# Kernel tuning notes

Measured on AMD Instinct MI355X. Metric: run time of the kernel, lower is better.

Reference implementation:

```python
import jax, jax.numpy as jnp
import numpy as np

# Static table layout: first N_NUM columns are numeric ('num:'), last N_CAT are categorical ('cat:').
B = 16384      # rows in the table
N_NUM = 32     # numeric columns
N_CAT = 8      # categorical columns
N_COLS = N_NUM + N_CAT
D = 256        # cell_embedding_dim
C = 16         # num_classes per categorical column = len(values) + 1 = 15 + 1


def setup_inputs() -> dict:
    key = jax.random.key(0)
    ks = jax.random.split(key, 7)
    s = 0.02  # typical init scale for Linear weights
    return {
        "cell_embeddings": jax.random.normal(ks[0], (B * N_COLS, D), dtype=jnp.float32),
        # numeric decoder: Linear(D, 1), stored as [D, 1] (transposed torch weight)
        "w_num": jax.random.normal(ks[1], (D, 1), dtype=jnp.float32) * s,
        "b_num": jnp.zeros((1,), dtype=jnp.float32),
        # categorical decoders: one Linear(D, C) per categorical column, stacked [N_CAT, D, C]
        "W_cat": jax.random.normal(ks[2], (N_CAT, D, C), dtype=jnp.float32) * s,
        "b_cat": jnp.zeros((N_CAT, C), dtype=jnp.float32),
        # missingness decoder: Linear(D, 1)
        "w_miss": jax.random.normal(ks[3], (D, 1), dtype=jnp.float32) * s,
        "b_miss": jnp.zeros((1,), dtype=jnp.float32),
    }


def reference(cell_embeddings, w_num, b_num, W_cat, b_cat, w_miss, b_miss):
    # [B*N_COLS, D] -> [B, N_COLS, D]; column j always routes to the same decoder.
    x = cell_embeddings.reshape(B, N_COLS, D)

    # Numeric cells: shared Linear(D -> 1), batched over all numeric cells.  [B, N_NUM]
    num_preds = (x[:, :N_NUM, :] @ w_num)[..., 0] + b_num[0]

    # Categorical cells: per-column Linear(D -> C), grouped GEMM.  [B, N_CAT, C]
    cat_logits = jnp.einsum('bjd,jdc->bjc', x[:, N_NUM:, :], W_cat) + b_cat

    # Missingness decoder applied to every cell.  [B, N_COLS]
    miss_logits = (x @ w_miss)[..., 0] + b_miss[0]

    return num_preds, cat_logits, miss_logits
```

## Files before the change

### kernel.cpp

```cpp
#include <hip/hip_runtime.h>

constexpr int B_     = 16384;
constexpr int NNUM   = 32;
constexpr int NCAT   = 8;
constexpr int NCOLS  = 40;
constexpr int DD     = 256;
constexpr int CC     = 16;

constexpr int BDIM     = 256;
constexpr int NBLOCKS  = 2048;
constexpr int NWAVES   = NBLOCKS * (BDIM / 64);
constexpr int NW_CAT   = 2048;
constexpr int NW_NUM   = NWAVES - NW_CAT;
constexpr int NUM_CELLS = B_ * NNUM;

constexpr int OUT_NUM_SZ  = B_ * NNUM;
constexpr int OUT_CAT_SZ  = B_ * NCAT * CC;

__global__ __launch_bounds__(BDIM, 4)
void tabdec_kernel(const float* __restrict__ X,
                   const float* __restrict__ w_num,  const float* __restrict__ b_num,
                   const float* __restrict__ W_cat,  const float* __restrict__ b_cat,
                   const float* __restrict__ w_miss, const float* __restrict__ b_miss,
                   float* __restrict__ out_num, float* __restrict__ out_cat,
                   float* __restrict__ out_miss)
{
    const int tid  = blockIdx.x * BDIM + threadIdx.x;
    const int wid  = tid >> 6;
    const int lane = threadIdx.x & 63;
    const float4* __restrict__ Xv = reinterpret_cast<const float4*>(X);

    if (wid < NW_NUM) {
        const float4 wn = reinterpret_cast<const float4*>(w_num)[lane];
        const float4 wm = reinterpret_cast<const float4*>(w_miss)[lane];
        const float bn = b_num[0];
        const float bm = b_miss[0];
        for (int i = 2 * wid; i < NUM_CELLS; i += 2 * NW_NUM) {
            const int b = i >> 5;
            const int j = i & 31;
            const int row0 = b * NCOLS + j;
            const float4 x0 = Xv[row0 * (DD / 4) + lane];
            const float4 x1 = Xv[(row0 + 1) * (DD / 4) + lane];
            float pn0 = x0.x * wn.x + x0.y * wn.y + x0.z * wn.z + x0.w * wn.w;
            float pm0 = x0.x * wm.x + x0.y * wm.y + x0.z * wm.z + x0.w * wm.w;
            float pn1 = x1.x * wn.x + x1.y * wn.y + x1.z * wn.z + x1.w * wn.w;
            float pm1 = x1.x * wm.x + x1.y * wm.y + x1.z * wm.z + x1.w * wm.w;
            #pragma unroll
            for (int m = 1; m < 64; m <<= 1) {
                pn0 += __shfl_xor(pn0, m, 64);
                pn1 += __shfl_xor(pn1, m, 64);
                pm0 += __shfl_xor(pm0, m, 64);
                pm1 += __shfl_xor(pm1, m, 64);
            }
            if (lane == 0) {
                out_num[i]     = pn0 + bn;
                out_num[i + 1] = pn1 + bn;
                out_miss[row0]     = pm0 + bm;
                out_miss[row0 + 1] = pm1 + bm;
            }
        }
    } else {
        const int wc = wid - NW_NUM;
        const int j  = wc >> 8;
        const int b0 = wc & 255;
        const float* Wj = W_cat + j * DD * CC;

        float4 w0[4], w1[4], w2[4], w3[4];
        #pragma unroll
        for (int k = 0; k < 4; ++k) {
            const float4* wr = reinterpret_cast<const float4*>(Wj + (lane * 4 + k) * CC);
            w0[k] = wr[0]; w1[k] = wr[1]; w2[k] = wr[2]; w3[k] = wr[3];
        }
        const float4 wm = reinterpret_cast<const float4*>(w_miss)[lane];
        const float bm = b_miss[0];
        const int cbr = ((lane & 1) << 3) | ((lane & 2) << 1) | ((lane & 4) >> 1) | ((lane & 8) >> 3);
        const float bias = b_cat[j * CC + cbr];
        const bool h1 = lane & 1, h2 = lane & 2, h3 = lane & 4, h4 = lane & 8;

        for (int b = b0; b < B_; b += 256) {
            const int row = b * NCOLS + NNUM + j;
            const float4 x = Xv[row * (DD / 4) + lane];
            const float xe0 = x.x, xe1 = x.y, xe2 = x.z, xe3 = x.w;

            float p[16];
            #pragma unroll
            for (int c = 0; c < 16; ++c) p[c] = 0.0f;
            #define ACC(k, xk) \
                p[0]  += xk * w0[k].x; p[1]  += xk * w0[k].y; p[2]  += xk * w0[k].z; p[3]  += xk * w0[k].w; \
                p[4]  += xk * w1[k].x; p[5]  += xk * w1[k].y; p[6]  += xk * w1[k].z; p[7]  += xk * w1[k].w; \
                p[8]  += xk * w2[k].x; p[9]  += xk * w2[k].y; p[10] += xk * w2[k].z; p[11] += xk * w2[k].w; \
                p[12] += xk * w3[k].x; p[13] += xk * w3[k].y; p[14] += xk * w3[k].z; p[15] += xk * w3[k].w;
            ACC(0, xe0) ACC(1, xe1) ACC(2, xe2) ACC(3, xe3)
            #undef ACC

            float pm = x.x * wm.x + x.y * wm.y + x.z * wm.z + x.w * wm.w;

            float q[8];
            #pragma unroll
            for (int i = 0; i < 8; ++i) {
                const float send = h1 ? p[i] : p[i + 8];
                const float keep = h1 ? p[i + 8] : p[i];
                q[i] = keep + __shfl_xor(send, 1, 64);
            }
            float r[4];
            #pragma unroll
            for (int i = 0; i < 4; ++i) {
                const float send = h2 ? q[i] : q[i + 4];
                const float keep = h2 ? q[i + 4] : q[i];
                r[i] = keep + __shfl_xor(send, 2, 64);
            }
            float s[2];
            #pragma unroll
            for (int i = 0; i < 2; ++i) {
                const float send = h3 ? r[i] : r[i + 2];
                const float keep = h3 ? r[i + 2] : r[i];
                s[i] = keep + __shfl_xor(send, 4, 64);
            }
            {
                const float send = h4 ? s[0] : s[1];
                const float keep = h4 ? s[1] : s[0];
                s[0] = keep + __shfl_xor(send, 8, 64);
            }
            float t = s[0];
            t += __shfl_xor(t, 16, 64);
            t += __shfl_xor(t, 32, 64);

            #pragma unroll
            for (int m = 1; m < 64; m <<= 1) pm += __shfl_xor(pm, m, 64);

            if (lane < 16) out_cat[b * (NCAT * CC) + j * CC + cbr] = t + bias;
            if (lane == 0) out_miss[b * NCOLS + NNUM + j] = pm + bm;
        }
    }
}

extern "C" void kernel_launch(void* const* d_in, const int* in_sizes, int n_in,
                              void* d_out, int out_size, void* d_ws, size_t ws_size,
                              hipStream_t stream) {
    const float* X      = (const float*)d_in[0];
    const float* w_num  = (const float*)d_in[1];
    const float* b_num  = (const float*)d_in[2];
    const float* W_cat  = (const float*)d_in[3];
    const float* b_cat  = (const float*)d_in[4];
    const float* w_miss = (const float*)d_in[5];
    const float* b_miss = (const float*)d_in[6];

    float* out_num  = (float*)d_out;
    float* out_cat  = out_num + OUT_NUM_SZ;
    float* out_miss = out_cat + OUT_CAT_SZ;

    tabdec_kernel<<<NBLOCKS, BDIM, 0, stream>>>(X, w_num, b_num, W_cat, b_cat,
                                                w_miss, b_miss,
                                                out_num, out_cat, out_miss);
}
```

Measured before the change: 891.4 us.

## Split decoder into separate numeric and categorical kernels with packed shuffle reduction

Replaces the single wave-partitioned kernel with two launches: a numeric kernel where each wave handles four cells and packs the num/miss dot products into one shared butterfly shuffle reduction, and a categorical kernel with twice as many waves per column. The aim is to cut shuffle count per cell and remove load imbalance between the two wave groups. In exchange the two phases now run serially on the stream, and the numeric kernel uses higher occupancy bounds.

Measured after the change: 883.0 us. About the same (-0.9%).

```diff
diff --git a/kernel.cpp b/kernel.cpp
--- a/kernel.cpp
+++ b/kernel.cpp
@@ -7,130 +7,153 @@
 constexpr int DD     = 256;
 constexpr int CC     = 16;
 
-constexpr int BDIM     = 256;
-constexpr int NBLOCKS  = 2048;
-constexpr int NWAVES   = NBLOCKS * (BDIM / 64);
-constexpr int NW_CAT   = 2048;
-constexpr int NW_NUM   = NWAVES - NW_CAT;
-constexpr int NUM_CELLS = B_ * NNUM;
-
 constexpr int OUT_NUM_SZ  = B_ * NNUM;
 constexpr int OUT_CAT_SZ  = B_ * NCAT * CC;
+constexpr int NUM_CELLS   = B_ * NNUM;
 
-__global__ __launch_bounds__(BDIM, 4)
-void tabdec_kernel(const float* __restrict__ X,
-                   const float* __restrict__ w_num,  const float* __restrict__ b_num,
-                   const float* __restrict__ W_cat,  const float* __restrict__ b_cat,
-                   const float* __restrict__ w_miss, const float* __restrict__ b_miss,
-                   float* __restrict__ out_num, float* __restrict__ out_cat,
-                   float* __restrict__ out_miss)
+constexpr int NB_NUM   = 2048;
+constexpr int NWAVE_N  = NB_NUM * 4;
+
+__global__ __launch_bounds__(256, 8)
+void tabdec_num(const float* __restrict__ X,
+                const float* __restrict__ w_num,  const float* __restrict__ b_num,
+                const float* __restrict__ w_miss, const float* __restrict__ b_miss,
+                float* __restrict__ out_num, float* __restrict__ out_miss)
 {
-    const int tid  = blockIdx.x * BDIM + threadIdx.x;
-    const int wid  = tid >> 6;
+    const int wid  = (blockIdx.x * 256 + threadIdx.x) >> 6;
     const int lane = threadIdx.x & 63;
     const float4* __restrict__ Xv = reinterpret_cast<const float4*>(X);
 
-    if (wid < NW_NUM) {
-        const float4 wn = reinterpret_cast<const float4*>(w_num)[lane];
-        const float4 wm = reinterpret_cast<const float4*>(w_miss)[lane];
-        const float bn = b_num[0];
-        const float bm = b_miss[0];
-        for (int i = 2 * wid; i < NUM_CELLS; i += 2 * NW_NUM) {
-            const int b = i >> 5;
-            const int j = i & 31;
-            const int row0 = b * NCOLS + j;
-            const float4 x0 = Xv[row0 * (DD / 4) + lane];
-            const float4 x1 = Xv[(row0 + 1) * (DD / 4) + lane];
-            float pn0 = x0.x * wn.x + x0.y * wn.y + x0.z * wn.z + x0.w * wn.w;
-            float pm0 = x0.x * wm.x + x0.y * wm.y + x0.z * wm.z + x0.w * wm.w;
-            float pn1 = x1.x * wn.x + x1.y * wn.y + x1.z * wn.z + x1.w * wn.w;
-            float pm1 = x1.x * wm.x + x1.y * wm.y + x1.z * wm.z + x1.w * wm.w;
-            #pragma unroll
-            for (int m = 1; m < 64; m <<= 1) {
-                pn0 += __shfl_xor(pn0, m, 64);
-                pn1 += __shfl_xor(pn1, m, 64);
-                pm0 += __shfl_xor(pm0, m, 64);
-                pm1 += __shfl_xor(pm1, m, 64);
-            }
-            if (lane == 0) {
-                out_num[i]     = pn0 + bn;
-                out_num[i + 1] = pn1 + bn;
-                out_miss[row0]     = pm0 + bm;
-                out_miss[row0 + 1] = pm1 + bm;
-            }
+    const float4 wn = reinterpret_cast<const float4*>(w_num)[lane];
+    const float4 wm = reinterpret_cast<const float4*>(w_miss)[lane];
+    const float bn = b_num[0];
+    const float bm = b_miss[0];
+
+    const bool bit0 = lane & 1, bit1 = lane & 2, bit2 = lane & 4;
+    const int cellsel = (lane >> 1) & 3;
+
+    for (int i = 4 * wid; i < NUM_CELLS; i += 4 * NWAVE_N) {
+        const int b    = i >> 5;
+        const int j    = i & 31;
+        const int row0 = b * NCOLS + j;
+
+        const float4 x0 = Xv[(row0 + 0) * (DD / 4) + lane];
+        const float4 x1 = Xv[(row0 + 1) * (DD / 4) + lane];
+        const float4 x2 = Xv[(row0 + 2) * (DD / 4) + lane];
+        const float4 x3 = Xv[(row0 + 3) * (DD / 4) + lane];
+
+        float pn0 = x0.x*wn.x + x0.y*wn.y + x0.z*wn.z + x0.w*wn.w;
+        float pm0 = x0.x*wm.x + x0.y*wm.y + x0.z*wm.z + x0.w*wm.w;
+        float pn1 = x1.x*wn.x + x1.y*wn.y + x1.z*wn.z + x1.w*wn.w;
+        float pm1 = x1.x*wm.x + x1.y*wm.y + x1.z*wm.z + x1.w*wm.w;
+        float pn2 = x2.x*wn.x + x2.y*wn.y + x2.z*wn.z + x2.w*wn.w;
+        float pm2 = x2.x*wm.x + x2.y*wm.y + x2.z*wm.z + x2.w*wm.w;
+        float pn3 = x3.x*wn.x + x3.y*wn.y + x3.z*wn.z + x3.w*wn.w;
+        float pm3 = x3.x*wm.x + x3.y*wm.y + x3.z*wm.z + x3.w*wm.w;
+
+        float q0, q1, q2, q3;
+        { float k0 = bit0 ? pm0 : pn0, s0 = bit0 ? pn0 : pm0; q0 = k0 + __shfl_xor(s0, 1, 64); }
+        { float k1 = bit0 ? pm1 : pn1, s1 = bit0 ? pn1 : pm1; q1 = k1 + __shfl_xor(s1, 1, 64); }
+        { float k2 = bit0 ? pm2 : pn2, s2 = bit0 ? pn2 : pm2; q2 = k2 + __shfl_xor(s2, 1, 64); }
+        { float k3 = bit0 ? pm3 : pn3, s3 = bit0 ? pn3 : pm3; q3 = k3 + __shfl_xor(s3, 1, 64); }
+        float r0, r1;
+        { float k = bit1 ? q0 : q1, kk = bit1 ? q1 : q0; r0 = kk + __shfl_xor(k, 2, 64); }
+        { float k = bit1 ? q2 : q3, kk = bit1 ? q3 : q2; r1 = kk + __shfl_xor(k, 2, 64); }
+        float s;
+        { float k = bit2 ? r0 : r1, kk = bit2 ? r1 : r0; s = kk + __shfl_xor(k, 4, 64); }
+        s += __shfl_xor(s, 8, 64);
+        s += __shfl_xor(s, 16, 64);
+        s += __shfl_xor(s, 32, 64);
+
+        if (lane < 8) {
+            if (!bit0) out_num[i + cellsel]     = s + bn;
+            else       out_miss[row0 + cellsel] = s + bm;
         }
-    } else {
-        const int wc = wid - NW_NUM;
-        const int j  = wc >> 8;
-        const int b0 = wc & 255;
-        const float* Wj = W_cat + j * DD * CC;
+    }
+}
 
-        float4 w0[4], w1[4], w2[4], w3[4];
+constexpr int NB_CAT  = 1024;
+constexpr int NWAVE_C = NB_CAT * 4;
+
+__global__ __launch_bounds__(256, 4)
+void tabdec_cat(const float* __restrict__ X,
+                const float* __restrict__ W_cat,  const float* __restrict__ b_cat,
+                const float* __restrict__ w_miss, const float* __restrict__ b_miss,
+                float* __restrict__ out_cat, float* __restrict__ out_miss)
+{
+    const int wid  = (blockIdx.x * 256 + threadIdx.x) >> 6;
+    const int lane = threadIdx.x & 63;
+    const float4* __restrict__ Xv = reinterpret_cast<const float4*>(X);
+
+    const int j  = wid >> 9;
+    const int b0 = wid & 511;
+    const float* Wj = W_cat + j * DD * CC;
+
+    float4 w0[4], w1[4], w2[4], w3[4];
+    #pragma unroll
+    for (int k = 0; k < 4; ++k) {
+        const float4* wr = reinterpret_cast<const float4*>(Wj + (lane * 4 + k) * CC);
+        w0[k] = wr[0]; w1[k] = wr[1]; w2[k] = wr[2]; w3[k] = wr[3];
+    }
+    const float4 wm = reinterpret_cast<const float4*>(w_miss)[lane];
+    const float bm = b_miss[0];
+    const int cbr = ((lane & 1) << 3) | ((lane & 2) << 1) | ((lane & 4) >> 1) | ((lane & 8) >> 3);
+    const float bias = b_cat[j * CC + cbr];
+    const bool h1 = lane & 1, h2 = lane & 2, h3 = lane & 4, h4 = lane & 8;
+
+    for (int b = b0; b < B_; b += 512) {
+        const int row = b * NCOLS + NNUM + j;
+        const float4 x = Xv[row * (DD / 4) + lane];
+        const float xe0 = x.x, xe1 = x.y, xe2 = x.z, xe3 = x.w;
+
+        float p[16];
         #pragma unroll
-        for (int k = 0; k < 4; ++k) {
-            const float4* wr = reinterpret_cast<const float4*>(Wj + (lane * 4 + k) * CC);
-            w0[k] = wr[0]; w1[k] = wr[1]; w2[k] = wr[2]; w3[k] = wr[3];
+        for (int c = 0; c < 16; ++c) p[c] = 0.0f;
+        #define ACC(k, xk) \
+            p[0]  += xk * w0[k].x; p[1]  += xk * w0[k].y; p[2]  += xk * w0[k].z; p[3]  += xk * w0[k].w; \
+            p[4]  += xk * w1[k].x; p[5]  += xk * w1[k].y; p[6]  += xk * w1[k].z; p[7]  += xk * w1[k].w; \
+            p[8]  += xk * w2[k].x; p[9]  += xk * w2[k].y; p[10] += xk * w2[k].z; p[11] += xk * w2[k].w; \
+            p[12] += xk * w3[k].x; p[13] += xk * w3[k].y; p[14] += xk * w3[k].z; p[15] += xk * w3[k].w;
+        ACC(0, xe0) ACC(1, xe1) ACC(2, xe2) ACC(3, xe3)
+        #undef ACC
+
+        float pm = x.x * wm.x + x.y * wm.y + x.z * wm.z + x.w * wm.w;
+
+        float q[8];
+        #pragma unroll
+        for (int i = 0; i < 8; ++i) {
+            const float send = h1 ? p[i] : p[i + 8];
+            const float keep = h1 ? p[i + 8] : p[i];
+            q[i] = keep + __shfl_xor(send, 1, 64);
         }
-        const float4 wm = reinterpret_cast<const float4*>(w_miss)[lane];
-        const float bm = b_miss[0];
-        const int cbr = ((lane & 1) << 3) | ((lane & 2) << 1) | ((lane & 4) >> 1) | ((lane & 8) >> 3);
-        const float bias = b_cat[j * CC + cbr];
-        const bool h1 = lane & 1, h2 = lane & 2, h3 = lane & 4, h4 = lane & 8;
+        float r[4];
+        #pragma unroll
+        for (int i = 0; i < 4; ++i) {
+            const float send = h2 ? q[i] : q[i + 4];
+            const float keep = h2 ? q[i + 4] : q[i];
+            r[i] = keep + __shfl_xor(send, 2, 64);
+        }
+        float ss[2];
+        #pragma unroll
+        for (int i = 0; i < 2; ++i) {
+            const float send = h3 ? r[i] : r[i + 2];
+            const float keep = h3 ? r[i + 2] : r[i];
+            ss[i] = keep + __shfl_xor(send, 4, 64);
+        }
+        {
+            const float send = h4 ? ss[0] : ss[1];
+            const float keep = h4 ? ss[1] : ss[0];
+            ss[0] = keep + __shfl_xor(send, 8, 64);
+        }
+        float t = ss[0];
+        t += __shfl_xor(t, 16, 64);
+        t += __shfl_xor(t, 32, 64);
 
-        for (int b = b0; b < B_; b += 256) {
-            const int row = b * NCOLS + NNUM + j;
-            const float4 x = Xv[row * (DD / 4) + lane];
-            const float xe0 = x.x, xe1 = x.y, xe2 = x.z, xe3 = x.w;
+        #pragma unroll
+        for (int m = 1; m < 64; m <<= 1) pm += __shfl_xor(pm, m, 64);
 
-            float p[16];
-            #pragma unroll
-            for (int c = 0; c < 16; ++c) p[c] = 0.0f;
-            #define ACC(k, xk) \
-                p[0]  += xk * w0[k].x; p[1]  += xk * w0[k].y; p[2]  += xk * w0[k].z; p[3]  += xk * w0[k].w; \
-                p[4]  += xk * w1[k].x; p[5]  += xk * w1[k].y; p[6]  += xk * w1[k].z; p[7]  += xk * w1[k].w; \
-                p[8]  += xk * w2[k].x; p[9]  += xk * w2[k].y; p[10] += xk * w2[k].z; p[11] += xk * w2[k].w; \
-                p[12] += xk * w3[k].x; p[13] += xk * w3[k].y; p[14] += xk * w3[k].z; p[15] += xk * w3[k].w;
-            ACC(0, xe0) ACC(1, xe1) ACC(2, xe2) ACC(3, xe3)
-            #undef ACC
-
-            float pm = x.x * wm.x + x.y * wm.y + x.z * wm.z + x.w * wm.w;
-
-            float q[8];
-            #pragma unroll
-            for (int i = 0; i < 8; ++i) {
-                const float send = h1 ? p[i] : p[i + 8];
-                const float keep = h1 ? p[i + 8] : p[i];
-                q[i] = keep + __shfl_xor(send, 1, 64);
-            }
-            float r[4];
-            #pragma unroll
-            for (int i = 0; i < 4; ++i) {
-                const float send = h2 ? q[i] : q[i + 4];
-                const float keep = h2 ? q[i + 4] : q[i];
-                r[i] = keep + __shfl_xor(send, 2, 64);
-            }
-            float s[2];
-            #pragma unroll
-            for (int i = 0; i < 2; ++i) {
-                const float send = h3 ? r[i] : r[i + 2];
-                const float keep = h3 ? r[i + 2] : r[i];
-                s[i] = keep + __shfl_xor(send, 4, 64);
-            }
-            {
-                const float send = h4 ? s[0] : s[1];
-                const float keep = h4 ? s[1] : s[0];
-                s[0] = keep + __shfl_xor(send, 8, 64);
-            }
-            float t = s[0];
-            t += __shfl_xor(t, 16, 64);
-            t += __shfl_xor(t, 32, 64);
-
-            #pragma unroll
-            for (int m = 1; m < 64; m <<= 1) pm += __shfl_xor(pm, m, 64);
-
-            if (lane < 16) out_cat[b * (NCAT * CC) + j * CC + cbr] = t + bias;
-            if (lane == 0) out_miss[b * NCOLS + NNUM + j] = pm + bm;
-        }
+        if (lane < 16) out_cat[b * (NCAT * CC) + j * CC + cbr] = t + bias;
+        if (lane == 0) out_miss[b * NCOLS + NNUM + j] = pm + bm;
     }
 }
 
@@ -149,7 +172,8 @@
     float* out_cat  = out_num + OUT_NUM_SZ;
     float* out_miss = out_cat + OUT_CAT_SZ;
 
-    tabdec_kernel<<<NBLOCKS, BDIM, 0, stream>>>(X, w_num, b_num, W_cat, b_cat,
-                                                w_miss, b_miss,
-                                                out_num, out_cat, out_miss);
+    tabdec_num<<<NB_NUM, 256, 0, stream>>>(X, w_num, b_num, w_miss, b_miss,
+                                           out_num, out_miss);
+    tabdec_cat<<<NB_CAT, 256, 0, stream>>>(X, W_cat, b_cat, w_miss, b_miss,
+                                           out_cat, out_miss);
 }
```
